# Kernel tuning notes

Hardware: AMD Instinct MI355X
Metric: run time of the kernel (lower is better)

## Reference

```python
import jax, jax.numpy as jnp
import numpy as np

AVG_NODES = 50.0  # matches init avg_nodes
EPS = 1e-9


def setup_inputs() -> dict:
    key = jax.random.key(0)
    k1, k2, k3 = jax.random.split(key, 3)
    N, D, G, OUT = 500000, 128, 10000, 128
    x = jax.random.normal(k1, (N, D), dtype=jnp.float32)
    batch = jnp.sort(jax.random.randint(k2, (N,), 0, G)).astype(jnp.int64)
    W = (jax.random.normal(k3, (5 * D, OUT), dtype=jnp.float32) / np.float32(np.sqrt(5 * D)))
    b = jnp.zeros((OUT,), dtype=jnp.float32)
    return {"x": x, "batch": batch, "W": W, "b": b, "num_segments": G}


def reference(x, batch, W, b, num_segments):
    G = num_segments  # static Python int
    N = x.shape[0]
    ones = jnp.ones((N,), dtype=x.dtype)
    counts = jnp.maximum(jax.ops.segment_sum(ones, batch, G), 1.0)[:, None]  # [G,1]
    x_sum = jax.ops.segment_sum(x, batch, G)            # [G,D]
    x_mean = x_sum / counts
    x_min = jax.ops.segment_min(x, batch, G)
    x_max = jax.ops.segment_max(x, batch, G)
    mean_sq = jax.ops.segment_sum(x * x, batch, G) / counts
    std = jnp.sqrt(jnp.maximum(mean_sq - x_mean ** 2, EPS))
    feats = jnp.concatenate(
        [x_sum * (1.0 / jnp.sqrt(jnp.float32(AVG_NODES))), x_mean, x_min, x_max, std],
        axis=1,
    )  # [G, 5D]
    return feats @ W + b
```

## Files before the change

kernel.cpp:

```cpp
#include <hip/hip_runtime.h>
#include <float.h>
#include <math.h>

#define D 128
#define FIVE_D 640
#define NOUT 128
#define ROWS 8

__global__ void seg_offsets_kernel(const int* __restrict__ batch, int* __restrict__ offs,
                                   int N, int G) {
    int g = blockIdx.x * blockDim.x + threadIdx.x;
    if (g > G) return;
    if (g == G) { offs[G] = N; return; }
    int lo = 0, hi = N;
    while (lo < hi) {
        int mid = (lo + hi) >> 1;
        if (batch[mid] < g) lo = mid + 1; else hi = mid;
    }
    offs[g] = lo;
}

__global__ __launch_bounds__(64) void seg_stats_kernel(const float* __restrict__ x,
                                                       const int* __restrict__ offs,
                                                       float* __restrict__ feats) {
    const int g = blockIdx.x;
    const int lane = threadIdx.x;
    const int start = offs[g];
    const int end   = offs[g + 1];

    float sx = 0.f, sy = 0.f, qx = 0.f, qy = 0.f;
    float mnx = FLT_MAX, mny = FLT_MAX, mxx = -FLT_MAX, mxy = -FLT_MAX;

    const float2* xp = reinterpret_cast<const float2*>(x) + lane;

    int r = start;
    for (; r + 2 <= end; r += 2) {
        float2 v0 = xp[r * 64];
        float2 v1 = xp[(r + 1) * 64];
        sx += v0.x; sy += v0.y;
        qx = fmaf(v0.x, v0.x, qx); qy = fmaf(v0.y, v0.y, qy);
        mnx = fminf(mnx, v0.x); mny = fminf(mny, v0.y);
        mxx = fmaxf(mxx, v0.x); mxy = fmaxf(mxy, v0.y);
        sx += v1.x; sy += v1.y;
        qx = fmaf(v1.x, v1.x, qx); qy = fmaf(v1.y, v1.y, qy);
        mnx = fminf(mnx, v1.x); mny = fminf(mny, v1.y);
        mxx = fmaxf(mxx, v1.x); mxy = fmaxf(mxy, v1.y);
    }
    if (r < end) {
        float2 v0 = xp[r * 64];
        sx += v0.x; sy += v0.y;
        qx = fmaf(v0.x, v0.x, qx); qy = fmaf(v0.y, v0.y, qy);
        mnx = fminf(mnx, v0.x); mny = fminf(mny, v0.y);
        mxx = fmaxf(mxx, v0.x); mxy = fmaxf(mxy, v0.y);
    }

    const float cnt = (float)max(end - start, 1);
    const float inv = 1.0f / cnt;
    const float meanx = sx * inv, meany = sy * inv;
    const float msqx = qx * inv, msqy = qy * inv;
    const float stdx = sqrtf(fmaxf(msqx - meanx * meanx, 1e-9f));
    const float stdy = sqrtf(fmaxf(msqy - meany * meany, 1e-9f));
    const float SC = 0.14142135623730950488f;

    float* f = feats + (size_t)g * FIVE_D + 2 * lane;
    f[0]         = sx * SC;  f[1]         = sy * SC;
    f[D]         = meanx;    f[D + 1]     = meany;
    f[2 * D]     = mnx;      f[2 * D + 1] = mny;
    f[3 * D]     = mxx;      f[3 * D + 1] = mxy;
    f[4 * D]     = stdx;     f[4 * D + 1] = stdy;
}

__global__ __launch_bounds__(64) void gemm_kernel(const float* __restrict__ feats,
                                                  const float* __restrict__ W,
                                                  const float* __restrict__ b,
                                                  float* __restrict__ out, int G) {
    __shared__ float lf[ROWS * FIVE_D];
    const int g0 = blockIdx.x * ROWS;
    const int lane = threadIdx.x;

    {
        const float4* src = reinterpret_cast<const float4*>(feats + (size_t)g0 * FIVE_D);
        float4* dst = reinterpret_cast<float4*>(lf);
        #pragma unroll
        for (int i = 0; i < (ROWS * FIVE_D) / 4 / 64; ++i)
            dst[i * 64 + lane] = src[i * 64 + lane];
    }
    __syncthreads();

    float acc0[ROWS], acc1[ROWS];
    #pragma unroll
    for (int r = 0; r < ROWS; ++r) { acc0[r] = 0.f; acc1[r] = 0.f; }

    for (int k = 0; k < FIVE_D; k += 4) {
        const float w00 = W[(k + 0) * NOUT + lane];
        const float w10 = W[(k + 0) * NOUT + 64 + lane];
        const float w01 = W[(k + 1) * NOUT + lane];
        const float w11 = W[(k + 1) * NOUT + 64 + lane];
        const float w02 = W[(k + 2) * NOUT + lane];
        const float w12 = W[(k + 2) * NOUT + 64 + lane];
        const float w03 = W[(k + 3) * NOUT + lane];
        const float w13 = W[(k + 3) * NOUT + 64 + lane];
        #pragma unroll
        for (int r = 0; r < ROWS; ++r) {
            const float4 f = *reinterpret_cast<const float4*>(&lf[r * FIVE_D + k]);
            acc0[r] = fmaf(f.x, w00, acc0[r]); acc1[r] = fmaf(f.x, w10, acc1[r]);
            acc0[r] = fmaf(f.y, w01, acc0[r]); acc1[r] = fmaf(f.y, w11, acc1[r]);
            acc0[r] = fmaf(f.z, w02, acc0[r]); acc1[r] = fmaf(f.z, w12, acc1[r]);
            acc0[r] = fmaf(f.w, w03, acc0[r]); acc1[r] = fmaf(f.w, w13, acc1[r]);
        }
    }

    const float b0 = b[lane];
    const float b1 = b[64 + lane];
    #pragma unroll
    for (int r = 0; r < ROWS; ++r) {
        const int g = g0 + r;
        if (g < G) {
            out[(size_t)g * NOUT + lane]      = acc0[r] + b0;
            out[(size_t)g * NOUT + 64 + lane] = acc1[r] + b1;
        }
    }
}

extern "C" void kernel_launch(void* const* d_in, const int* in_sizes, int n_in,
                              void* d_out, int out_size, void* d_ws, size_t ws_size,
                              hipStream_t stream) {
    const float* x     = (const float*)d_in[0];
    const int*   batch = (const int*)d_in[1];
    const float* W     = (const float*)d_in[2];
    const float* b     = (const float*)d_in[3];
    float* out = (float*)d_out;

    const int N = in_sizes[0] / D;
    const int G = out_size / NOUT;

    int*   offs  = (int*)d_ws;
    float* feats = (float*)((char*)d_ws + 65536);

    seg_offsets_kernel<<<(G + 1 + 255) / 256, 256, 0, stream>>>(batch, offs, N, G);
    seg_stats_kernel<<<G, 64, 0, stream>>>(x, offs, feats);
    gemm_kernel<<<(G + ROWS - 1) / ROWS, 64, 0, stream>>>(feats, W, b, out, G);
}
```

Before: 455.8 us.

## Use float4 row-pair loads in segment stats and split GEMM rows across four waves

The stats kernel now has each half-wave read one full row with float4 loads and handles two rows per step, unrolled by four. The two halves are merged with cross-lane shuffles and written back as float4 stores. The GEMM kernel uses 256 threads per block, with each wave computing two of the eight rows, so each wave does less serial work and more waves are available. The cost is that every wave reloads W, which multiplies global or L2 traffic for W by four per block.

```diff
diff --git a/kernel.cpp b/kernel.cpp
--- a/kernel.cpp
+++ b/kernel.cpp
@@ -5,7 +5,7 @@
 #define D 128
 #define FIVE_D 640
 #define NOUT 128
-#define ROWS 8
+#define GR 8
 
 __global__ void seg_offsets_kernel(const int* __restrict__ batch, int* __restrict__ offs,
                                    int N, int G) {
@@ -25,100 +25,127 @@
                                                        float* __restrict__ feats) {
     const int g = blockIdx.x;
     const int lane = threadIdx.x;
+    const int half = lane >> 5;
+    const int c = lane & 31;
     const int start = offs[g];
     const int end   = offs[g + 1];
 
-    float sx = 0.f, sy = 0.f, qx = 0.f, qy = 0.f;
-    float mnx = FLT_MAX, mny = FLT_MAX, mxx = -FLT_MAX, mxy = -FLT_MAX;
+    float4 s  = make_float4(0.f, 0.f, 0.f, 0.f);
+    float4 q  = make_float4(0.f, 0.f, 0.f, 0.f);
+    float4 mn = make_float4(FLT_MAX, FLT_MAX, FLT_MAX, FLT_MAX);
+    float4 mx = make_float4(-FLT_MAX, -FLT_MAX, -FLT_MAX, -FLT_MAX);
 
-    const float2* xp = reinterpret_cast<const float2*>(x) + lane;
+    const float4* xp = reinterpret_cast<const float4*>(x) + c;
 
-    int r = start;
-    for (; r + 2 <= end; r += 2) {
-        float2 v0 = xp[r * 64];
-        float2 v1 = xp[(r + 1) * 64];
-        sx += v0.x; sy += v0.y;
-        qx = fmaf(v0.x, v0.x, qx); qy = fmaf(v0.y, v0.y, qy);
-        mnx = fminf(mnx, v0.x); mny = fminf(mny, v0.y);
-        mxx = fmaxf(mxx, v0.x); mxy = fmaxf(mxy, v0.y);
-        sx += v1.x; sy += v1.y;
-        qx = fmaf(v1.x, v1.x, qx); qy = fmaf(v1.y, v1.y, qy);
-        mnx = fminf(mnx, v1.x); mny = fminf(mny, v1.y);
-        mxx = fmaxf(mxx, v1.x); mxy = fmaxf(mxy, v1.y);
+    auto acc = [&](float4 v) {
+        s.x += v.x; s.y += v.y; s.z += v.z; s.w += v.w;
+        q.x = fmaf(v.x, v.x, q.x); q.y = fmaf(v.y, v.y, q.y);
+        q.z = fmaf(v.z, v.z, q.z); q.w = fmaf(v.w, v.w, q.w);
+        mn.x = fminf(mn.x, v.x); mn.y = fminf(mn.y, v.y);
+        mn.z = fminf(mn.z, v.z); mn.w = fminf(mn.w, v.w);
+        mx.x = fmaxf(mx.x, v.x); mx.y = fmaxf(mx.y, v.y);
+        mx.z = fmaxf(mx.z, v.z); mx.w = fmaxf(mx.w, v.w);
+    };
+
+    int base = start;
+    for (; base + 8 <= end; base += 8) {
+        float4 v0 = xp[(size_t)(base + 0 + half) * 32];
+        float4 v1 = xp[(size_t)(base + 2 + half) * 32];
+        float4 v2 = xp[(size_t)(base + 4 + half) * 32];
+        float4 v3 = xp[(size_t)(base + 6 + half) * 32];
+        acc(v0); acc(v1); acc(v2); acc(v3);
     }
-    if (r < end) {
-        float2 v0 = xp[r * 64];
-        sx += v0.x; sy += v0.y;
-        qx = fmaf(v0.x, v0.x, qx); qy = fmaf(v0.y, v0.y, qy);
-        mnx = fminf(mnx, v0.x); mny = fminf(mny, v0.y);
-        mxx = fmaxf(mxx, v0.x); mxy = fmaxf(mxy, v0.y);
+    for (; base + 2 <= end; base += 2) {
+        float4 v = xp[(size_t)(base + half) * 32];
+        acc(v);
+    }
+    if (base < end && half == 0) {
+        float4 v = xp[(size_t)base * 32];
+        acc(v);
     }
 
-    const float cnt = (float)max(end - start, 1);
-    const float inv = 1.0f / cnt;
-    const float meanx = sx * inv, meany = sy * inv;
-    const float msqx = qx * inv, msqy = qy * inv;
-    const float stdx = sqrtf(fmaxf(msqx - meanx * meanx, 1e-9f));
-    const float stdy = sqrtf(fmaxf(msqy - meany * meany, 1e-9f));
-    const float SC = 0.14142135623730950488f;
+    s.x += __shfl_xor(s.x, 32); s.y += __shfl_xor(s.y, 32);
+    s.z += __shfl_xor(s.z, 32); s.w += __shfl_xor(s.w, 32);
+    q.x += __shfl_xor(q.x, 32); q.y += __shfl_xor(q.y, 32);
+    q.z += __shfl_xor(q.z, 32); q.w += __shfl_xor(q.w, 32);
+    mn.x = fminf(mn.x, __shfl_xor(mn.x, 32)); mn.y = fminf(mn.y, __shfl_xor(mn.y, 32));
+    mn.z = fminf(mn.z, __shfl_xor(mn.z, 32)); mn.w = fminf(mn.w, __shfl_xor(mn.w, 32));
+    mx.x = fmaxf(mx.x, __shfl_xor(mx.x, 32)); mx.y = fmaxf(mx.y, __shfl_xor(mx.y, 32));
+    mx.z = fmaxf(mx.z, __shfl_xor(mx.z, 32)); mx.w = fmaxf(mx.w, __shfl_xor(mx.w, 32));
 
-    float* f = feats + (size_t)g * FIVE_D + 2 * lane;
-    f[0]         = sx * SC;  f[1]         = sy * SC;
-    f[D]         = meanx;    f[D + 1]     = meany;
-    f[2 * D]     = mnx;      f[2 * D + 1] = mny;
-    f[3 * D]     = mxx;      f[3 * D + 1] = mxy;
-    f[4 * D]     = stdx;     f[4 * D + 1] = stdy;
+    if (half == 0) {
+        const float cnt = (float)max(end - start, 1);
+        const float inv = 1.0f / cnt;
+        const float SC = 0.14142135623730950488f;
+        float4 mean = make_float4(s.x * inv, s.y * inv, s.z * inv, s.w * inv);
+        float4 sd;
+        sd.x = sqrtf(fmaxf(q.x * inv - mean.x * mean.x, 1e-9f));
+        sd.y = sqrtf(fmaxf(q.y * inv - mean.y * mean.y, 1e-9f));
+        sd.z = sqrtf(fmaxf(q.z * inv - mean.z * mean.z, 1e-9f));
+        sd.w = sqrtf(fmaxf(q.w * inv - mean.w * mean.w, 1e-9f));
+        float4 ssc = make_float4(s.x * SC, s.y * SC, s.z * SC, s.w * SC);
+
+        float* f = feats + (size_t)g * FIVE_D + 4 * c;
+        *reinterpret_cast<float4*>(f)         = ssc;
+        *reinterpret_cast<float4*>(f + D)     = mean;
+        *reinterpret_cast<float4*>(f + 2 * D) = mn;
+        *reinterpret_cast<float4*>(f + 3 * D) = mx;
+        *reinterpret_cast<float4*>(f + 4 * D) = sd;
+    }
 }
 
-__global__ __launch_bounds__(64) void gemm_kernel(const float* __restrict__ feats,
-                                                  const float* __restrict__ W,
-                                                  const float* __restrict__ b,
-                                                  float* __restrict__ out, int G) {
-    __shared__ float lf[ROWS * FIVE_D];
-    const int g0 = blockIdx.x * ROWS;
-    const int lane = threadIdx.x;
+__global__ __launch_bounds__(256) void gemm_kernel(const float* __restrict__ feats,
+                                                   const float* __restrict__ W,
+                                                   const float* __restrict__ b,
+                                                   float* __restrict__ out, int G) {
+    __shared__ float lf[GR * FIVE_D];
+    const int tid = threadIdx.x;
+    const int lane = tid & 63;
+    const int wave = tid >> 6;
+    const int g0 = blockIdx.x * GR;
 
     {
         const float4* src = reinterpret_cast<const float4*>(feats + (size_t)g0 * FIVE_D);
         float4* dst = reinterpret_cast<float4*>(lf);
         #pragma unroll
-        for (int i = 0; i < (ROWS * FIVE_D) / 4 / 64; ++i)
-            dst[i * 64 + lane] = src[i * 64 + lane];
+        for (int i = 0; i < (GR * FIVE_D) / 4 / 256; ++i)
+            dst[i * 256 + tid] = src[i * 256 + tid];
     }
     __syncthreads();
 
-    float acc0[ROWS], acc1[ROWS];
-    #pragma unroll
-    for (int r = 0; r < ROWS; ++r) { acc0[r] = 0.f; acc1[r] = 0.f; }
+    const int r0 = wave * 2, r1 = wave * 2 + 1;
+    float a00 = 0.f, a01 = 0.f, a10 = 0.f, a11 = 0.f;
 
     for (int k = 0; k < FIVE_D; k += 4) {
         const float w00 = W[(k + 0) * NOUT + lane];
-        const float w10 = W[(k + 0) * NOUT + 64 + lane];
-        const float w01 = W[(k + 1) * NOUT + lane];
+        const float w01 = W[(k + 0) * NOUT + 64 + lane];
+        const float w10 = W[(k + 1) * NOUT + lane];
         const float w11 = W[(k + 1) * NOUT + 64 + lane];
-        const float w02 = W[(k + 2) * NOUT + lane];
-        const float w12 = W[(k + 2) * NOUT + 64 + lane];
-        const float w03 = W[(k + 3) * NOUT + lane];
-        const float w13 = W[(k + 3) * NOUT + 64 + lane];
-        #pragma unroll
-        for (int r = 0; r < ROWS; ++r) {
-            const float4 f = *reinterpret_cast<const float4*>(&lf[r * FIVE_D + k]);
-            acc0[r] = fmaf(f.x, w00, acc0[r]); acc1[r] = fmaf(f.x, w10, acc1[r]);
-            acc0[r] = fmaf(f.y, w01, acc0[r]); acc1[r] = fmaf(f.y, w11, acc1[r]);
-            acc0[r] = fmaf(f.z, w02, acc0[r]); acc1[r] = fmaf(f.z, w12, acc1[r]);
-            acc0[r] = fmaf(f.w, w03, acc0[r]); acc1[r] = fmaf(f.w, w13, acc1[r]);
-        }
+        const float w20 = W[(k + 2) * NOUT + lane];
+        const float w21 = W[(k + 2) * NOUT + 64 + lane];
+        const float w30 = W[(k + 3) * NOUT + lane];
+        const float w31 = W[(k + 3) * NOUT + 64 + lane];
+        const float4 f0 = *reinterpret_cast<const float4*>(&lf[r0 * FIVE_D + k]);
+        const float4 f1 = *reinterpret_cast<const float4*>(&lf[r1 * FIVE_D + k]);
+        a00 = fmaf(f0.x, w00, a00); a01 = fmaf(f0.x, w01, a01);
+        a10 = fmaf(f1.x, w00, a10); a11 = fmaf(f1.x, w01, a11);
+        a00 = fmaf(f0.y, w10, a00); a01 = fmaf(f0.y, w11, a01);
+        a10 = fmaf(f1.y, w10, a10); a11 = fmaf(f1.y, w11, a11);
+        a00 = fmaf(f0.z, w20, a00); a01 = fmaf(f0.z, w21, a01);
+        a10 = fmaf(f1.z, w20, a10); a11 = fmaf(f1.z, w21, a11);
+        a00 = fmaf(f0.w, w30, a00); a01 = fmaf(f0.w, w31, a01);
+        a10 = fmaf(f1.w, w30, a10); a11 = fmaf(f1.w, w31, a11);
     }
 
     const float b0 = b[lane];
     const float b1 = b[64 + lane];
-    #pragma unroll
-    for (int r = 0; r < ROWS; ++r) {
-        const int g = g0 + r;
-        if (g < G) {
-            out[(size_t)g * NOUT + lane]      = acc0[r] + b0;
-            out[(size_t)g * NOUT + 64 + lane] = acc1[r] + b1;
-        }
+    if (g0 + r0 < G) {
+        out[(size_t)(g0 + r0) * NOUT + lane]      = a00 + b0;
+        out[(size_t)(g0 + r0) * NOUT + 64 + lane] = a01 + b1;
+    }
+    if (g0 + r1 < G) {
+        out[(size_t)(g0 + r1) * NOUT + lane]      = a10 + b0;
+        out[(size_t)(g0 + r1) * NOUT + 64 + lane] = a11 + b1;
     }
 }
 
@@ -139,5 +166,5 @@
 
     seg_offsets_kernel<<<(G + 1 + 255) / 256, 256, 0, stream>>>(batch, offs, N, G);
     seg_stats_kernel<<<G, 64, 0, stream>>>(x, offs, feats);
-    gemm_kernel<<<(G + ROWS - 1) / ROWS, 64, 0, stream>>>(feats, W, b, out, G);
+    gemm_kernel<<<(G + GR - 1) / GR, 256, 0, stream>>>(feats, W, b, out, G);
 }
```

Result: faster. 425.5 us (-6.6%).
